# Performance work log

Measured on AMD Instinct MI355X. Metric: run time of the kernel, lower is better.

The kernel has to match this reference:

```python
import jax, jax.numpy as jnp
import numpy as np

SR = 4  # search_range
D = 2 * SR + 1  # 9
NC = D * D      # 81 output channels


def setup_inputs() -> dict:
    key = jax.random.key(0)
    k1, k2 = jax.random.split(key)
    B, C, H, W = 8, 64, 192, 256
    x1 = jax.random.normal(k1, (B, C, H, W), dtype=jnp.float32)
    x2 = jax.random.normal(k2, (B, C, H, W), dtype=jnp.float32)
    return {"x1": x1, "x2": x2}


def reference(x1, x2):
    B, C, H, W = x1.shape
    # Zero-pad x2 so out-of-overlap products are zero, matching the
    # zero-initialized cv in the original module.
    x2p = jnp.pad(x2, ((0, 0), (0, 0), (SR, SR), (SR, SR)))
    outs = [None] * NC
    for i in range(-SR, SR + 1):
        for j in range(-SR, SR + 1):
            # Original torch code uses cv[:, 9*i + j] with negative wraparound.
            k = (D * i + j) % NC
            # x2 sample position is (h - i, w - j); in padded coords start = SR - i.
            shifted = jax.lax.dynamic_slice(
                x2p, (0, 0, SR - i, SR - j), (B, C, H, W))
            outs[k] = jnp.sum(x1 * shifted, axis=1)  # [B, H, W]
    cv = jnp.stack(outs, axis=1)  # [B, 81, H, W]
    return cv / NC
```

## Files before the change

kernel.cpp:

```cpp
#include <hip/hip_runtime.h>

#define HH 192
#define WW 256
#define TH 8
#define TW 32
#define CCH 8
#define NCHUNK 8
#define THREADS 576
#define CHSTEP (CCH * HH * WW)

typedef float f4 __attribute__((ext_vector_type(4)));

#define GLL(gp, lp) __builtin_amdgcn_global_load_lds(                        \
    (const __attribute__((address_space(1))) unsigned int*)(gp),            \
    (__attribute__((address_space(3))) unsigned int*)(lp), 16, 0, 0)

__global__ __launch_bounds__(THREADS) void cost_volume_kernel(
    const float* __restrict__ x1, const float* __restrict__ x2,
    float* __restrict__ out)
{
    __shared__ __align__(16) float smem[20480];

    const int tid  = threadIdx.x;
    const int wave = tid >> 6;
    const int lane = tid & 63;
    const int r    = lane >> 3;
    const int wcg  = lane & 7;

    const int bid = blockIdx.x;
    const int b   = bid / 192;
    const int rem = bid % 192;
    const int h0  = (rem >> 3) * TH;
    const int w0  = (rem & 7) * TW;

    auto desc2 = [&](int u, bool& v, int& goff) {
        const int ch = u >> 8, row = (u >> 4) & 15, cu = u & 15;
        const int hg = h0 - 4 + row, wg = w0 - 4 + cu * 4;
        v = (cu <= 9) & (hg >= 0) & (hg < HH) & (wg >= 0) & (wg <= WW - 4);
        goff = ((b * 64 + ch) * HH + hg) * WW + wg;
    };
    const int sA = wave, sB = wave + 9, sC = wave + 18, sD = wave + 27;
    bool vA, vB, vC, vD0; int gA, gB, gC, gD;
    desc2((sA << 6) + lane, vA, gA);
    desc2((sB << 6) + lane, vB, gB);
    desc2((sC << 6) + lane, vC, gC);
    desc2(((sD & 31) << 6) + lane, vD0, gD);
    const bool vD = vD0 & (wave < 5);

    const bool v1 = (wave < 8);
    const int u1 = ((wave & 7) << 6) + lane;
    const int ch1 = u1 >> 6, r1 = (u1 >> 3) & 7, c1 = (u1 & 7) * 4;
    const int g1 = ((b * 64 + ch1) * HH + (h0 + r1)) * WW + (w0 + c1);

    auto issue = [&](int nb, int n) {
        const int cofs = n * CHSTEP;
        float* const b2 = smem + 4096 + nb * 8192;
        float* const b1 = smem + nb * 2048;
        if (vA) GLL(x2 + gA + cofs, b2 + (sA << 8));
        if (vB) GLL(x2 + gB + cofs, b2 + (sB << 8));
        if (vC) GLL(x2 + gC + cofs, b2 + (sC << 8));
        if (vD) GLL(x2 + gD + cofs, b2 + (sD << 8));
        if (v1) GLL(x1 + g1 + cofs, b1 + ((wave & 7) << 8));
    };

    const f4 z4 = {0.f, 0.f, 0.f, 0.f};
    for (int z = tid; z < 20480 / 4; z += THREADS) ((f4*)smem)[z] = z4;
    __syncthreads();

    issue(0, 0);
    __syncthreads();

    f4 acc0 = z4, acc1 = z4, acc2 = z4, acc3 = z4, acc4 = z4,
       acc5 = z4, acc6 = z4, acc7 = z4, acc8 = z4;

    const int row2 = r + 8 - wave;

    for (int n = 0; n < NCHUNK; ++n) {
        if (n + 1 < NCHUNK) issue((n + 1) & 1, n + 1);
        const float* sb1 = smem + (n & 1) * 2048 + r * 32 + wcg * 4;
        const float* sb2 = smem + 4096 + (n & 1) * 8192 + row2 * 64 + wcg * 4;
#pragma unroll
        for (int cc = 0; cc < CCH; ++cc) {
            const f4 av  = *(const f4*)(sb1 + cc * 256);
            const f4 xv0 = *(const f4*)(sb2 + cc * 1024);
            const f4 xv1 = *(const f4*)(sb2 + cc * 1024 + 4);
            const f4 xv2 = *(const f4*)(sb2 + cc * 1024 + 8);
            const f4 w8 = xv0;
            const f4 w7 = __builtin_shufflevector(xv0, xv1, 1, 2, 3, 4);
            const f4 w6 = __builtin_shufflevector(xv0, xv1, 2, 3, 4, 5);
            const f4 w5 = __builtin_shufflevector(xv0, xv1, 3, 4, 5, 6);
            const f4 w4 = xv1;
            const f4 w3 = __builtin_shufflevector(xv1, xv2, 1, 2, 3, 4);
            const f4 w2 = __builtin_shufflevector(xv1, xv2, 2, 3, 4, 5);
            const f4 w1w = __builtin_shufflevector(xv1, xv2, 3, 4, 5, 6);
            const f4 w0w = xv2;
            acc0 = __builtin_elementwise_fma(av, w0w, acc0);
            acc1 = __builtin_elementwise_fma(av, w1w, acc1);
            acc2 = __builtin_elementwise_fma(av, w2, acc2);
            acc3 = __builtin_elementwise_fma(av, w3, acc3);
            acc4 = __builtin_elementwise_fma(av, w4, acc4);
            acc5 = __builtin_elementwise_fma(av, w5, acc5);
            acc6 = __builtin_elementwise_fma(av, w6, acc6);
            acc7 = __builtin_elementwise_fma(av, w7, acc7);
            acc8 = __builtin_elementwise_fma(av, w8, acc8);
        }
        __syncthreads();
    }

    const float scale = 1.0f / 81.0f;
    const int hout = h0 + r;
    const int wout = w0 + wcg * 4;
#define CV_OUT(JJ)                                                           \
    {                                                                        \
        const int k = (9 * wave + (JJ) + 41) % 81;                           \
        float* po = out + ((b * 81 + k) * HH + hout) * WW + wout;            \
        *(f4*)po = acc##JJ * scale;                                          \
    }
    CV_OUT(0) CV_OUT(1) CV_OUT(2) CV_OUT(3) CV_OUT(4)
    CV_OUT(5) CV_OUT(6) CV_OUT(7) CV_OUT(8)
#undef CV_OUT
}

extern "C" void kernel_launch(void* const* d_in, const int* in_sizes, int n_in,
                              void* d_out, int out_size, void* d_ws, size_t ws_size,
                              hipStream_t stream) {
    const float* x1 = (const float*)d_in[0];
    const float* x2 = (const float*)d_in[1];
    float* out = (float*)d_out;
    dim3 grid(8 * 24 * 8);
    dim3 block(THREADS);
    hipLaunchKernelGGL(cost_volume_kernel, grid, block, 0, stream, x1, x2, out);
}
```

Measured before the change: 112.5 us.

## Reshape cost-volume tile to 4x64 with compact 18-column LDS halo layout

```diff
diff --git a/kernel.cpp b/kernel.cpp
--- a/kernel.cpp
+++ b/kernel.cpp
@@ -2,12 +2,20 @@
 
 #define HH 192
 #define WW 256
-#define TH 8
-#define TW 32
+#define TH 4
+#define TW 64
 #define CCH 8
 #define NCHUNK 8
 #define THREADS 576
 #define CHSTEP (CCH * HH * WW)
+
+#define X2_RU   18
+#define X2_ROWS 12
+#define X2_CHF  (X2_ROWS * X2_RU * 4)
+#define BUFF2   (CCH * X2_CHF)
+#define X1_CHF  (TH * TW)
+#define BUFF1   (CCH * X1_CHF)
+#define S1_OFF  (2 * BUFF2)
 
 typedef float f4 __attribute__((ext_vector_type(4)));
 
@@ -19,52 +27,51 @@
     const float* __restrict__ x1, const float* __restrict__ x2,
     float* __restrict__ out)
 {
-    __shared__ __align__(16) float smem[20480];
+    __shared__ __align__(16) float smem[2 * BUFF2 + 2 * BUFF1];
 
     const int tid  = threadIdx.x;
     const int wave = tid >> 6;
     const int lane = tid & 63;
-    const int r    = lane >> 3;
-    const int wcg  = lane & 7;
+    const int r    = lane >> 4;
+    const int wcg  = lane & 15;
 
     const int bid = blockIdx.x;
     const int b   = bid / 192;
     const int rem = bid % 192;
-    const int h0  = (rem >> 3) * TH;
-    const int w0  = (rem & 7) * TW;
+    const int h0  = (rem >> 2) * TH;
+    const int w0  = (rem & 3) * TW;
 
-    auto desc2 = [&](int u, bool& v, int& goff) {
-        const int ch = u >> 8, row = (u >> 4) & 15, cu = u & 15;
-        const int hg = h0 - 4 + row, wg = w0 - 4 + cu * 4;
-        v = (cu <= 9) & (hg >= 0) & (hg < HH) & (wg >= 0) & (wg <= WW - 4);
-        goff = ((b * 64 + ch) * HH + hg) * WW + wg;
+    auto desc2 = [&](int s, int& goff) {
+        const int u = (s << 6) + lane;
+        const int ch = u / 216, rm = u % 216;
+        const int row = rm / 18, cu = rm % 18;
+        const int hg = h0 - 4 + row, wg = w0 - 4 + (cu << 2);
+        const bool v = (hg >= 0) & (hg < HH) & (wg >= 0) & (wg <= WW - 4);
+        goff = v ? (((b * 64 + ch) * HH + hg) * WW + wg) : -1;
     };
-    const int sA = wave, sB = wave + 9, sC = wave + 18, sD = wave + 27;
-    bool vA, vB, vC, vD0; int gA, gB, gC, gD;
-    desc2((sA << 6) + lane, vA, gA);
-    desc2((sB << 6) + lane, vB, gB);
-    desc2((sC << 6) + lane, vC, gC);
-    desc2(((sD & 31) << 6) + lane, vD0, gD);
-    const bool vD = vD0 & (wave < 5);
+    int gA, gB, gC;
+    desc2(wave, gA);
+    desc2(wave + 9, gB);
+    desc2(wave + 18, gC);
 
-    const bool v1 = (wave < 8);
-    const int u1 = ((wave & 7) << 6) + lane;
-    const int ch1 = u1 >> 6, r1 = (u1 >> 3) & 7, c1 = (u1 & 7) * 4;
-    const int g1 = ((b * 64 + ch1) * HH + (h0 + r1)) * WW + (w0 + c1);
+    const bool v1 = (wave >= 1);
+    const int s1 = (wave - 1) & 7;
+    const int g1 = ((b * 64 + s1) * HH + (h0 + (lane >> 4))) * WW +
+                   w0 + ((lane & 15) << 2);
 
     auto issue = [&](int nb, int n) {
         const int cofs = n * CHSTEP;
-        float* const b2 = smem + 4096 + nb * 8192;
-        float* const b1 = smem + nb * 2048;
-        if (vA) GLL(x2 + gA + cofs, b2 + (sA << 8));
-        if (vB) GLL(x2 + gB + cofs, b2 + (sB << 8));
-        if (vC) GLL(x2 + gC + cofs, b2 + (sC << 8));
-        if (vD) GLL(x2 + gD + cofs, b2 + (sD << 8));
-        if (v1) GLL(x1 + g1 + cofs, b1 + ((wave & 7) << 8));
+        float* const b2 = smem + nb * BUFF2;
+        float* const b1 = smem + S1_OFF + nb * BUFF1;
+        if (gA >= 0) GLL(x2 + gA + cofs, b2 + (wave << 8));
+        if (gB >= 0) GLL(x2 + gB + cofs, b2 + ((wave + 9) << 8));
+        if (gC >= 0) GLL(x2 + gC + cofs, b2 + ((wave + 18) << 8));
+        if (v1)      GLL(x1 + g1 + cofs, b1 + (s1 << 8));
     };
 
     const f4 z4 = {0.f, 0.f, 0.f, 0.f};
-    for (int z = tid; z < 20480 / 4; z += THREADS) ((f4*)smem)[z] = z4;
+    for (int z = tid; z < (2 * BUFF2 + 2 * BUFF1) / 4; z += THREADS)
+        ((f4*)smem)[z] = z4;
     __syncthreads();
 
     issue(0, 0);
@@ -77,14 +84,14 @@
 
     for (int n = 0; n < NCHUNK; ++n) {
         if (n + 1 < NCHUNK) issue((n + 1) & 1, n + 1);
-        const float* sb1 = smem + (n & 1) * 2048 + r * 32 + wcg * 4;
-        const float* sb2 = smem + 4096 + (n & 1) * 8192 + row2 * 64 + wcg * 4;
+        const float* sb2 = smem + (n & 1) * BUFF2 + row2 * (X2_RU * 4) + (wcg << 2);
+        const float* sb1 = smem + S1_OFF + (n & 1) * BUFF1 + r * TW + (wcg << 2);
 #pragma unroll
         for (int cc = 0; cc < CCH; ++cc) {
-            const f4 av  = *(const f4*)(sb1 + cc * 256);
-            const f4 xv0 = *(const f4*)(sb2 + cc * 1024);
-            const f4 xv1 = *(const f4*)(sb2 + cc * 1024 + 4);
-            const f4 xv2 = *(const f4*)(sb2 + cc * 1024 + 8);
+            const f4 av  = *(const f4*)(sb1 + cc * X1_CHF);
+            const f4 xv0 = *(const f4*)(sb2 + cc * X2_CHF);
+            const f4 xv1 = *(const f4*)(sb2 + cc * X2_CHF + 4);
+            const f4 xv2 = *(const f4*)(sb2 + cc * X2_CHF + 8);
             const f4 w8 = xv0;
             const f4 w7 = __builtin_shufflevector(xv0, xv1, 1, 2, 3, 4);
             const f4 w6 = __builtin_shufflevector(xv0, xv1, 2, 3, 4, 5);
@@ -109,11 +116,11 @@
 
     const float scale = 1.0f / 81.0f;
     const int hout = h0 + r;
-    const int wout = w0 + wcg * 4;
+    const int wout = w0 + (wcg << 2);
 #define CV_OUT(JJ)                                                           \
     {                                                                        \
         const int k = (9 * wave + (JJ) + 41) % 81;                           \
-        float* po = out + ((b * 81 + k) * HH + hout) * WW + wout;            \
+        float* po = out + (((long)b * 81 + k) * HH + hout) * WW + wout;      \
         *(f4*)po = acc##JJ * scale;                                          \
     }
     CV_OUT(0) CV_OUT(1) CV_OUT(2) CV_OUT(3) CV_OUT(4)
@@ -127,7 +134,7 @@
     const float* x1 = (const float*)d_in[0];
     const float* x2 = (const float*)d_in[1];
     float* out = (float*)d_out;
-    dim3 grid(8 * 24 * 8);
+    dim3 grid(8 * 48 * 4);
     dim3 block(THREADS);
     hipLaunchKernelGGL(cost_volume_kernel, grid, block, 0, stream, x1, x2, out);
 }
```

Result: no change. 114.0 us (+1.3%).
